# Optimization experiments

Hardware: AMD Instinct MI355X
Metric: run time of the kernel (lower is better)

The kernel has to match this reference:

```python
import jax, jax.numpy as jnp
import numpy as np

B, C_IN, C_OUT, H, W = 8, 4, 64, 8, 2048


def setup_inputs() -> dict:
    key = jax.random.key(0)
    ks = jax.random.split(key, 7)
    # torch Conv2d default init: U(-s, s) with s = 1/sqrt(fan_in), fan_in = C_in*1*1
    s = 1.0 / np.sqrt(C_IN)
    u = lambda k, shape: jax.random.uniform(k, shape, jnp.float32, -s, s)
    return {
        "x": jax.random.normal(ks[0], (B, C_IN, H, W), jnp.float32),
        "Wq": u(ks[1], (C_OUT, C_IN)), "bq": u(ks[2], (C_OUT,)),
        "Wk": u(ks[3], (C_OUT, C_IN)), "bk": u(ks[4], (C_OUT,)),
        "Wv": u(ks[5], (C_OUT, C_IN)), "bv": u(ks[6], (C_OUT,)),
        "causal": 1,
    }


def reference(x, Wq, bq, Wk, bk, Wv, bv, causal):
    b, c_in, h, w = x.shape
    # 1x1 conv == per-pixel linear over channel axis
    def proj(Wm, bm):
        y = jnp.einsum('bchw,oc->bohw', x, Wm) + bm[None, :, None, None]
        return y.reshape(b, -1, w)              # [B, C_out*H, W]
    Q = proj(Wq, bq)
    K = proj(Wk, bk)
    V = proj(Wv, bv)
    d = Q.shape[1]
    # scores[b,k,l] = sum_d Q[b,d,k] * K[b,d,l] / sqrt(d)   -> [B, W, W]
    scores = jnp.einsum('bdk,bdl->bkl', Q, K) / (float(d) ** 0.5)
    if causal:
        # faithful to torch: triu zeros lower triangle, then any zero -> -inf
        scores = jnp.triu(scores)
        scores = jnp.where(scores != 0, scores, -jnp.inf)
    attn = jax.nn.softmax(scores, axis=-1)
    # x_out[b,d,k] = sum_l V[b,d,l] * attn[b,k,l]
    x_out = jnp.einsum('bdl,bkl->bdk', V, attn).reshape(b, -1, h, w)
    return x_out, scores  # plot_weight is the pre-softmax (masked) scores
```

## Files before the change

### kernel.cpp

```cpp
#include <hip/hip_runtime.h>
#include <math.h>


#define B_ 8
#define W_ 2048
#define D_ 512
#define SCALE_ 0.04419417382415922f
#define NEG_BIG_ (-3.0e38f)

typedef __attribute__((ext_vector_type(8))) short bf16x8;
typedef __attribute__((ext_vector_type(4))) float f32x4;

__device__ __forceinline__ unsigned short f2bf(float x) {
  unsigned int u = __float_as_uint(x);
  u += 0x7fffu + ((u >> 16) & 1u);
  return (unsigned short)(u >> 16);
}
__device__ __forceinline__ float bf2f(unsigned short h) {
  return __uint_as_float(((unsigned int)h) << 16);
}
__device__ __forceinline__ void split2(float x, unsigned short& hi, unsigned short& lo) {
  hi = f2bf(x);
  lo = f2bf(x - bf2f(hi));
}

__device__ __forceinline__ void gl16(const unsigned short* g, unsigned short* l) {
  __builtin_amdgcn_global_load_lds(
      (__attribute__((address_space(1))) void*)const_cast<unsigned short*>(g),
      (__attribute__((address_space(3))) void*)l, 16, 0, 0);
}

__device__ __forceinline__ int swz(int row, int lq) {
  return row * 32 + ((lq ^ ((row >> 1) & 3)) << 3);
}

__global__ __launch_bounds__(256) void proj_all(
    const float* __restrict__ x,
    const float* __restrict__ Wq, const float* __restrict__ bq,
    const float* __restrict__ Wk, const float* __restrict__ bk,
    const float* __restrict__ Wv, const float* __restrict__ bv,
    unsigned short* __restrict__ Qhi, unsigned short* __restrict__ Qlo,
    unsigned short* __restrict__ Khi, unsigned short* __restrict__ Klo,
    unsigned short* __restrict__ Vhi, unsigned short* __restrict__ Vlo) {
  int bid = blockIdx.x;
  if (bid < 4096) {
    int idx = bid * 256 + threadIdx.x;
    int o = idx & 63;
    int w = (idx >> 6) & (W_ - 1);
    int b = idx >> 17;
    const float* xb = x + (size_t)b * 32 * W_ + w;
    float xv[4][8];
#pragma unroll
    for (int c = 0; c < 4; c++)
#pragma unroll
      for (int h = 0; h < 8; h++) xv[c][h] = xb[(c * 8 + h) * W_];
    float wq0 = Wq[o * 4], wq1 = Wq[o * 4 + 1], wq2 = Wq[o * 4 + 2], wq3 = Wq[o * 4 + 3];
    float wk0 = Wk[o * 4], wk1 = Wk[o * 4 + 1], wk2 = Wk[o * 4 + 2], wk3 = Wk[o * 4 + 3];
    float bqv = bq[o], bkv = bk[o];
    unsigned short qh8[8] __attribute__((aligned(16))), ql8[8] __attribute__((aligned(16)));
    unsigned short kh8[8] __attribute__((aligned(16))), kl8[8] __attribute__((aligned(16)));
#pragma unroll
    for (int h = 0; h < 8; h++) {
      float q = bqv + wq0 * xv[0][h] + wq1 * xv[1][h] + wq2 * xv[2][h] + wq3 * xv[3][h];
      float k = bkv + wk0 * xv[0][h] + wk1 * xv[1][h] + wk2 * xv[2][h] + wk3 * xv[3][h];
      split2(q, qh8[h], ql8[h]);
      split2(k, kh8[h], kl8[h]);
    }
    size_t base = ((size_t)b * W_ + w) * D_ + o * 8;
    *(uint4*)&Qhi[base] = *(uint4*)qh8;
    *(uint4*)&Qlo[base] = *(uint4*)ql8;
    *(uint4*)&Khi[base] = *(uint4*)kh8;
    *(uint4*)&Klo[base] = *(uint4*)kl8;
  } else {
    int idx = (bid - 4096) * 256 + threadIdx.x;
    int wc = idx & 255;
    int d = (idx >> 8) & (D_ - 1);
    int b = idx >> 17;
    int o = d >> 3, h = d & 7;
    const float* xp = x + ((size_t)(b * 4) * 8 + h) * W_ + wc * 8;
    float4 xa[4][2];
#pragma unroll
    for (int c = 0; c < 4; c++) {
      xa[c][0] = *(const float4*)&xp[(size_t)c * 8 * W_];
      xa[c][1] = *(const float4*)&xp[(size_t)c * 8 * W_ + 4];
    }
    float w0 = Wv[o * 4], w1 = Wv[o * 4 + 1], w2 = Wv[o * 4 + 2], w3 = Wv[o * 4 + 3];
    float bvv = bv[o];
    unsigned short vh8[8] __attribute__((aligned(16))), vl8[8] __attribute__((aligned(16)));
#pragma unroll
    for (int j = 0; j < 8; j++) {
      float x0 = (j < 4) ? ((const float*)&xa[0][0])[j] : ((const float*)&xa[0][1])[j - 4];
      float x1 = (j < 4) ? ((const float*)&xa[1][0])[j] : ((const float*)&xa[1][1])[j - 4];
      float x2 = (j < 4) ? ((const float*)&xa[2][0])[j] : ((const float*)&xa[2][1])[j - 4];
      float x3 = (j < 4) ? ((const float*)&xa[3][0])[j] : ((const float*)&xa[3][1])[j - 4];
      float v = bvv + w0 * x0 + w1 * x1 + w2 * x2 + w3 * x3;
      split2(v, vh8[j], vl8[j]);
    }
    size_t base = ((size_t)b * D_ + d) * W_ + wc * 8;
    *(uint4*)&Vhi[base] = *(uint4*)vh8;
    *(uint4*)&Vlo[base] = *(uint4*)vl8;
  }
}

__global__ __launch_bounds__(256) void scores_mfma(
    const unsigned short* __restrict__ Qhi, const unsigned short* __restrict__ Qlo,
    const unsigned short* __restrict__ Khi, const unsigned short* __restrict__ Klo,
    float* __restrict__ S, float2* __restrict__ stats, const int* __restrict__ causal_p) {
  int f = (blockIdx.z * 16 + blockIdx.y) * 16 + blockIdx.x;
  int lf = (f & 7) * 256 + (f >> 3);
  int b = lf >> 8;
  int k0 = ((lf >> 4) & 15) * 128;
  int l0 = (lf & 15) * 128;
  int causal = *causal_p;
  int t = threadIdx.x;
  float* Sb = S + (size_t)b * W_ * W_;

  if (causal && (l0 + 127 < k0)) {
    float4 nb = make_float4(NEG_BIG_, NEG_BIG_, NEG_BIG_, NEG_BIG_);
    int row = t >> 1, c0 = (t & 1) * 64;
#pragma unroll
    for (int j = 0; j < 16; j++)
      *(float4*)&Sb[(size_t)(k0 + row) * W_ + l0 + c0 + j * 4] = nb;
    return;
  }

  __shared__ __align__(16) unsigned short qh_s[2][4096], ql_s[2][4096];
  __shared__ __align__(16) unsigned short kh_s[2][4096], kl_s[2][4096];
  __shared__ float sm_h[2][128], ss_h[2][128];

  int wave = t >> 6, lane = t & 63;
  int wk0 = (wave >> 1) * 64, wl0 = (wave & 1) * 64;
  int lr = lane & 15, lq = lane >> 4;

  const unsigned short* Qhb = Qhi + ((size_t)b * W_ + k0) * D_;
  const unsigned short* Qlb = Qlo + ((size_t)b * W_ + k0) * D_;
  const unsigned short* Khb = Khi + ((size_t)b * W_ + l0) * D_;
  const unsigned short* Klb = Klo + ((size_t)b * W_ + l0) * D_;

  int srow0 = t >> 2, sq = t & 3;
  int srow1 = srow0 + 64;
  size_t g0 = (size_t)srow0 * D_ + ((sq ^ ((srow0 >> 1) & 3)) << 3);
  size_t g1 = (size_t)srow1 * D_ + ((sq ^ ((srow1 >> 1) & 3)) << 3);
  int a0 = t * 8, a1 = t * 8 + 2048;

  auto stage = [&](int buf, int d0) {
    gl16(Qhb + g0 + d0, &qh_s[buf][a0]);
    gl16(Qhb + g1 + d0, &qh_s[buf][a1]);
    gl16(Qlb + g0 + d0, &ql_s[buf][a0]);
    gl16(Qlb + g1 + d0, &ql_s[buf][a1]);
    gl16(Khb + g0 + d0, &kh_s[buf][a0]);
    gl16(Khb + g1 + d0, &kh_s[buf][a1]);
    gl16(Klb + g0 + d0, &kl_s[buf][a0]);
    gl16(Klb + g1 + d0, &kl_s[buf][a1]);
  };

  f32x4 acc[4][4];
#pragma unroll
  for (int i = 0; i < 4; i++)
#pragma unroll
    for (int j = 0; j < 4; j++) acc[i][j] = (f32x4){0.f, 0.f, 0.f, 0.f};

  stage(0, 0);
  __syncthreads();

  for (int i = 0; i < 16; i++) {
    int cur = i & 1;
    if (i < 15) stage(cur ^ 1, (i + 1) * 32);

    bf16x8 ah[4], al[4], bh[4], bl[4];
#pragma unroll
    for (int mt = 0; mt < 4; mt++) {
      int a = swz(wk0 + mt * 16 + lr, lq);
      ah[mt] = *(const bf16x8*)&qh_s[cur][a];
      al[mt] = *(const bf16x8*)&ql_s[cur][a];
    }
#pragma unroll
    for (int nt = 0; nt < 4; nt++) {
      int a = swz(wl0 + nt * 16 + lr, lq);
      bh[nt] = *(const bf16x8*)&kh_s[cur][a];
      bl[nt] = *(const bf16x8*)&kl_s[cur][a];
    }
    __builtin_amdgcn_s_setprio(1);
#pragma unroll
    for (int mt = 0; mt < 4; mt++)
#pragma unroll
      for (int nt = 0; nt < 4; nt++) {
        acc[mt][nt] = __builtin_amdgcn_mfma_f32_16x16x32_bf16(ah[mt], bh[nt], acc[mt][nt], 0, 0, 0);
        acc[mt][nt] = __builtin_amdgcn_mfma_f32_16x16x32_bf16(ah[mt], bl[nt], acc[mt][nt], 0, 0, 0);
        acc[mt][nt] = __builtin_amdgcn_mfma_f32_16x16x32_bf16(al[mt], bh[nt], acc[mt][nt], 0, 0, 0);
      }
    __builtin_amdgcn_s_setprio(0);
    __syncthreads();
  }

  int wh = wl0 >> 6;
#pragma unroll
  for (int mt = 0; mt < 4; mt++)
#pragma unroll
    for (int r = 0; r < 4; r++) {
      int rr = wk0 + mt * 16 + lq * 4 + r;
      int k = k0 + rr;
      float v4[4];
#pragma unroll
      for (int nt = 0; nt < 4; nt++) {
        int l = l0 + wl0 + nt * 16 + lr;
        float s = acc[mt][nt][r] * SCALE_;
        if (causal && (l < k || s == 0.0f)) s = NEG_BIG_;
        Sb[(size_t)k * W_ + l] = s;
        v4[nt] = s;
      }
      float mx = fmaxf(fmaxf(v4[0], v4[1]), fmaxf(v4[2], v4[3]));
#pragma unroll
      for (int off = 1; off < 16; off <<= 1) mx = fmaxf(mx, __shfl_xor(mx, off, 64));
      float ss = __expf(v4[0] - mx) + __expf(v4[1] - mx) +
                 __expf(v4[2] - mx) + __expf(v4[3] - mx);
#pragma unroll
      for (int off = 1; off < 16; off <<= 1) ss += __shfl_xor(ss, off, 64);
      if (lr == 0) { sm_h[wh][rr] = mx; ss_h[wh][rr] = ss; }
    }
  __syncthreads();
  if (t < 128) {
    float m0 = sm_h[0][t], m1 = sm_h[1][t];
    float s0 = ss_h[0][t], s1 = ss_h[1][t];
    float m = fmaxf(m0, m1);
    float ssum = s0 * __expf(m0 - m) + s1 * __expf(m1 - m);
    stats[((size_t)b * W_ + k0 + t) * 16 + (l0 >> 7)] = make_float2(m, ssum);
  }
}

__global__ __launch_bounds__(256) void out_bal(
    const unsigned short* __restrict__ Vhi, const unsigned short* __restrict__ Vlo,
    const float* __restrict__ S, const float2* __restrict__ stats,
    float* __restrict__ O, const int* __restrict__ causal_p) {
  int f = blockIdx.z * 64 + blockIdx.x;
  int lf = (f & 7) * 64 + (f >> 3);
  int b = lf >> 6;
  int j2 = lf & 63;
  int k0 = (j2 >> 2) * 128;
  int dq = j2 & 3;
  int causal = *causal_p;
  int t = threadIdx.x;
  int wave = t >> 6, lane = t & 63;
  int wd0 = (wave >> 1) * 64;
  int wk0 = (wave & 1) * 64;
  int lr = lane & 15, lq = lane >> 4;

  __shared__ __align__(16) unsigned short vh_s[2][128 * 32], vl_s[2][128 * 32];
  __shared__ __align__(16) unsigned short ph_s[2][128 * 32], pl_s[2][128 * 32];

  const unsigned short* Vhb = Vhi + ((size_t)b * D_ + dq * 128) * W_;
  const unsigned short* Vlb = Vlo + ((size_t)b * D_ + dq * 128) * W_;
  const float* Sb = S + (size_t)b * W_ * W_;

  int rA = t >> 2, qc = t & 3;
  int vx = (qc ^ ((rA >> 1) & 3)) << 3;
  const unsigned short* VhA = Vhb + (size_t)rA * W_ + vx;
  const unsigned short* VhB = VhA + (size_t)64 * W_;
  const unsigned short* VlA = Vlb + (size_t)rA * W_ + vx;
  const unsigned short* VlB = VlA + (size_t)64 * W_;
  int a0 = t * 8, a1 = t * 8 + 2048;

  const float* SrowA = Sb + (size_t)(k0 + rA) * W_ + qc * 8;
  const float* SrowB = SrowA + (size_t)64 * W_;
  int pA = rA * 32 + vx;
  int pB = pA + 64 * 32;

  int lt0 = causal ? (k0 >> 7) : 0;
  const float2* spA = stats + ((size_t)b * W_ + k0 + rA) * 16;
  const float2* spB = spA + 64 * 16;
  float mA = -INFINITY, mB = -INFINITY;
  for (int lt = lt0; lt < 16; lt++) mA = fmaxf(mA, spA[lt].x);
  for (int lt = lt0; lt < 16; lt++) mB = fmaxf(mB, spB[lt].x);
  float sA = 0.f, sB = 0.f;
  for (int lt = lt0; lt < 16; lt++) sA += spA[lt].y * __expf(spA[lt].x - mA);
  for (int lt = lt0; lt < 16; lt++) sB += spB[lt].y * __expf(spB[lt].x - mB);
  float iA = 1.0f / sA, iB = 1.0f / sB;

  f32x4 acc[4][4];
#pragma unroll
  for (int i = 0; i < 4; i++)
#pragma unroll
    for (int j = 0; j < 4; j++) acc[i][j] = (f32x4){0.f, 0.f, 0.f, 0.f};

  int lstart = causal ? k0 : 0;
  int nch = (W_ - lstart) >> 5;

  auto stageV = [&](int buf, int l) {
    gl16(VhA + l, &vh_s[buf][a0]);
    gl16(VhB + l, &vh_s[buf][a1]);
    gl16(VlA + l, &vl_s[buf][a0]);
    gl16(VlB + l, &vl_s[buf][a1]);
  };
  auto writeP = [&](unsigned short* __restrict__ ph, unsigned short* __restrict__ pl,
                    float4 sa0, float4 sa1, float4 sb0, float4 sb1) {
    float p[8];
    unsigned short hi8[8] __attribute__((aligned(16)));
    unsigned short lo8[8] __attribute__((aligned(16)));
    p[0] = __expf(sa0.x - mA) * iA; p[1] = __expf(sa0.y - mA) * iA;
    p[2] = __expf(sa0.z - mA) * iA; p[3] = __expf(sa0.w - mA) * iA;
    p[4] = __expf(sa1.x - mA) * iA; p[5] = __expf(sa1.y - mA) * iA;
    p[6] = __expf(sa1.z - mA) * iA; p[7] = __expf(sa1.w - mA) * iA;
#pragma unroll
    for (int j = 0; j < 8; j++) split2(p[j], hi8[j], lo8[j]);
    *(uint4*)&ph[pA] = *(uint4*)hi8;
    *(uint4*)&pl[pA] = *(uint4*)lo8;
    p[0] = __expf(sb0.x - mB) * iB; p[1] = __expf(sb0.y - mB) * iB;
    p[2] = __expf(sb0.z - mB) * iB; p[3] = __expf(sb0.w - mB) * iB;
    p[4] = __expf(sb1.x - mB) * iB; p[5] = __expf(sb1.y - mB) * iB;
    p[6] = __expf(sb1.z - mB) * iB; p[7] = __expf(sb1.w - mB) * iB;
#pragma unroll
    for (int j = 0; j < 8; j++) split2(p[j], hi8[j], lo8[j]);
    *(uint4*)&ph[pB] = *(uint4*)hi8;
    *(uint4*)&pl[pB] = *(uint4*)lo8;
  };
  auto compute = [&](const unsigned short* vh, const unsigned short* vl,
                     const unsigned short* ph, const unsigned short* pl) {
    bf16x8 ah[4], al[4], bh[4], bl[4];
#pragma unroll
    for (int mt = 0; mt < 4; mt++) {
      int a = swz(wd0 + mt * 16 + lr, lq);
      ah[mt] = *(const bf16x8*)&vh[a];
      al[mt] = *(const bf16x8*)&vl[a];
    }
#pragma unroll
    for (int nt = 0; nt < 4; nt++) {
      int a = swz(wk0 + nt * 16 + lr, lq);
      bh[nt] = *(const bf16x8*)&ph[a];
      bl[nt] = *(const bf16x8*)&pl[a];
    }
    __builtin_amdgcn_s_setprio(1);
#pragma unroll
    for (int mt = 0; mt < 4; mt++)
#pragma unroll
      for (int nt = 0; nt < 4; nt++) {
        acc[mt][nt] = __builtin_amdgcn_mfma_f32_16x16x32_bf16(ah[mt], bh[nt], acc[mt][nt], 0, 0, 0);
        acc[mt][nt] = __builtin_amdgcn_mfma_f32_16x16x32_bf16(ah[mt], bl[nt], acc[mt][nt], 0, 0, 0);
        acc[mt][nt] = __builtin_amdgcn_mfma_f32_16x16x32_bf16(al[mt], bh[nt], acc[mt][nt], 0, 0, 0);
      }
    __builtin_amdgcn_s_setprio(0);
  };

  float4 sAE0, sAE1, sBE0, sBE1, sAO0, sAO1, sBO0, sBO1;

  sAE0 = *(const float4*)&SrowA[lstart];      sAE1 = *(const float4*)&SrowA[lstart + 4];
  sBE0 = *(const float4*)&SrowB[lstart];      sBE1 = *(const float4*)&SrowB[lstart + 4];
  sAO0 = *(const float4*)&SrowA[lstart + 32]; sAO1 = *(const float4*)&SrowA[lstart + 36];
  sBO0 = *(const float4*)&SrowB[lstart + 32]; sBO1 = *(const float4*)&SrowB[lstart + 36];
  stageV(0, lstart);
  writeP(&ph_s[0][0], &pl_s[0][0], sAE0, sAE1, sBE0, sBE1);
  __syncthreads();

  for (int ci = 0; ci < nch; ci += 2) {
    int base = lstart + ci * 32;
    if (ci + 2 < nch) {
      sAE0 = *(const float4*)&SrowA[base + 64]; sAE1 = *(const float4*)&SrowA[base + 68];
      sBE0 = *(const float4*)&SrowB[base + 64]; sBE1 = *(const float4*)&SrowB[base + 68];
    }
    stageV(1, base + 32);
    writeP(&ph_s[1][0], &pl_s[1][0], sAO0, sAO1, sBO0, sBO1);
    compute(&vh_s[0][0], &vl_s[0][0], &ph_s[0][0], &pl_s[0][0]);
    __syncthreads();
    bool more = (ci + 2 < nch);
    if (ci + 3 < nch) {
      sAO0 = *(const float4*)&SrowA[base + 96]; sAO1 = *(const float4*)&SrowA[base + 100];
      sBO0 = *(const float4*)&SrowB[base + 96]; sBO1 = *(const float4*)&SrowB[base + 100];
    }
    if (more) {
      stageV(0, base + 64);
      writeP(&ph_s[0][0], &pl_s[0][0], sAE0, sAE1, sBE0, sBE1);
    }
    compute(&vh_s[1][0], &vl_s[1][0], &ph_s[1][0], &pl_s[1][0]);
    __syncthreads();
  }

#pragma unroll
  for (int mt = 0; mt < 4; mt++)
#pragma unroll
    for (int nt = 0; nt < 4; nt++)
#pragma unroll
      for (int r = 0; r < 4; r++) {
        int d = dq * 128 + wd0 + mt * 16 + lq * 4 + r;
        int k = k0 + wk0 + nt * 16 + lr;
        O[((size_t)b * D_ + d) * W_ + k] = acc[mt][nt][r];
      }
}

extern "C" void kernel_launch(void* const* d_in, const int* in_sizes, int n_in,
                              void* d_out, int out_size, void* d_ws, size_t ws_size,
                              hipStream_t stream) {
  const float* x  = (const float*)d_in[0];
  const float* Wq = (const float*)d_in[1];
  const float* bq = (const float*)d_in[2];
  const float* Wk = (const float*)d_in[3];
  const float* bk = (const float*)d_in[4];
  const float* Wv = (const float*)d_in[5];
  const float* bv = (const float*)d_in[6];
  const int* causal = (const int*)d_in[7];

  float* out = (float*)d_out;
  float* x_out = out;
  float* S = out + (size_t)B_ * D_ * W_;

  const size_t NQ = (size_t)B_ * W_ * D_;
  unsigned short* wsu = (unsigned short*)d_ws;
  unsigned short* Qhi = wsu;
  unsigned short* Qlo = wsu + NQ;
  unsigned short* Khi = wsu + 2 * NQ;
  unsigned short* Klo = wsu + 3 * NQ;
  unsigned short* Vhi = wsu + 4 * NQ;
  unsigned short* Vlo = wsu + 5 * NQ;
  float2* stats = (float2*)(wsu + 6 * NQ);

  proj_all<<<8192, 256, 0, stream>>>(x, Wq, bq, Wk, bk, Wv, bv,
                                     Qhi, Qlo, Khi, Klo, Vhi, Vlo);
  scores_mfma<<<dim3(16, 16, B_), 256, 0, stream>>>(Qhi, Qlo, Khi, Klo, S, stats, causal);
  out_bal<<<dim3(64, 1, B_), 256, 0, stream>>>(Vhi, Vlo, S, stats, x_out, causal);
}
```

Before: 371.7 us.

## Triple-buffer V loads with partial vmcnt waits; single-buffer score-kernel LDS

```diff
diff --git a/kernel.cpp b/kernel.cpp
--- a/kernel.cpp
+++ b/kernel.cpp
@@ -33,6 +33,9 @@
 __device__ __forceinline__ int swz(int row, int lq) {
   return row * 32 + ((lq ^ ((row >> 1) & 3)) << 3);
 }
+
+#define BAR_KEEP8() asm volatile("s_waitcnt vmcnt(8) lgkmcnt(0)\n\ts_barrier" ::: "memory")
+#define BAR_DRAIN() asm volatile("s_waitcnt vmcnt(0) lgkmcnt(0)\n\ts_barrier" ::: "memory")
 
 __global__ __launch_bounds__(256) void proj_all(
     const float* __restrict__ x,
@@ -124,8 +127,8 @@
     return;
   }
 
-  __shared__ __align__(16) unsigned short qh_s[2][4096], ql_s[2][4096];
-  __shared__ __align__(16) unsigned short kh_s[2][4096], kl_s[2][4096];
+  __shared__ __align__(16) unsigned short qh_s[128 * 32], ql_s[128 * 32];
+  __shared__ __align__(16) unsigned short kh_s[128 * 32], kl_s[128 * 32];
   __shared__ float sm_h[2][128], ss_h[2][128];
 
   int wave = t >> 6, lane = t & 63;
@@ -143,42 +146,35 @@
   size_t g1 = (size_t)srow1 * D_ + ((sq ^ ((srow1 >> 1) & 3)) << 3);
   int a0 = t * 8, a1 = t * 8 + 2048;
 
-  auto stage = [&](int buf, int d0) {
-    gl16(Qhb + g0 + d0, &qh_s[buf][a0]);
-    gl16(Qhb + g1 + d0, &qh_s[buf][a1]);
-    gl16(Qlb + g0 + d0, &ql_s[buf][a0]);
-    gl16(Qlb + g1 + d0, &ql_s[buf][a1]);
-    gl16(Khb + g0 + d0, &kh_s[buf][a0]);
-    gl16(Khb + g1 + d0, &kh_s[buf][a1]);
-    gl16(Klb + g0 + d0, &kl_s[buf][a0]);
-    gl16(Klb + g1 + d0, &kl_s[buf][a1]);
-  };
-
   f32x4 acc[4][4];
 #pragma unroll
   for (int i = 0; i < 4; i++)
 #pragma unroll
     for (int j = 0; j < 4; j++) acc[i][j] = (f32x4){0.f, 0.f, 0.f, 0.f};
 
-  stage(0, 0);
-  __syncthreads();
-
-  for (int i = 0; i < 16; i++) {
-    int cur = i & 1;
-    if (i < 15) stage(cur ^ 1, (i + 1) * 32);
+  for (int d0 = 0; d0 < D_; d0 += 32) {
+    gl16(Qhb + g0 + d0, &qh_s[a0]);
+    gl16(Qhb + g1 + d0, &qh_s[a1]);
+    gl16(Qlb + g0 + d0, &ql_s[a0]);
+    gl16(Qlb + g1 + d0, &ql_s[a1]);
+    gl16(Khb + g0 + d0, &kh_s[a0]);
+    gl16(Khb + g1 + d0, &kh_s[a1]);
+    gl16(Klb + g0 + d0, &kl_s[a0]);
+    gl16(Klb + g1 + d0, &kl_s[a1]);
+    __syncthreads();
 
     bf16x8 ah[4], al[4], bh[4], bl[4];
 #pragma unroll
     for (int mt = 0; mt < 4; mt++) {
       int a = swz(wk0 + mt * 16 + lr, lq);
-      ah[mt] = *(const bf16x8*)&qh_s[cur][a];
-      al[mt] = *(const bf16x8*)&ql_s[cur][a];
+      ah[mt] = *(const bf16x8*)&qh_s[a];
+      al[mt] = *(const bf16x8*)&ql_s[a];
     }
 #pragma unroll
     for (int nt = 0; nt < 4; nt++) {
       int a = swz(wl0 + nt * 16 + lr, lq);
-      bh[nt] = *(const bf16x8*)&kh_s[cur][a];
-      bl[nt] = *(const bf16x8*)&kl_s[cur][a];
+      bh[nt] = *(const bf16x8*)&kh_s[a];
+      bl[nt] = *(const bf16x8*)&kl_s[a];
     }
     __builtin_amdgcn_s_setprio(1);
 #pragma unroll
@@ -245,8 +241,8 @@
   int wk0 = (wave & 1) * 64;
   int lr = lane & 15, lq = lane >> 4;
 
-  __shared__ __align__(16) unsigned short vh_s[2][128 * 32], vl_s[2][128 * 32];
-  __shared__ __align__(16) unsigned short ph_s[2][128 * 32], pl_s[2][128 * 32];
+  __shared__ __align__(16) unsigned short vh_s[3][4096], vl_s[3][4096];
+  __shared__ __align__(16) unsigned short ph_s[2][4096], pl_s[2][4096];
 
   const unsigned short* Vhb = Vhi + ((size_t)b * D_ + dq * 128) * W_;
   const unsigned short* Vlb = Vlo + ((size_t)b * D_ + dq * 128) * W_;
@@ -285,11 +281,16 @@
   int lstart = causal ? k0 : 0;
   int nch = (W_ - lstart) >> 5;
 
-  auto stageV = [&](int buf, int l) {
-    gl16(VhA + l, &vh_s[buf][a0]);
-    gl16(VhB + l, &vh_s[buf][a1]);
-    gl16(VlA + l, &vl_s[buf][a0]);
-    gl16(VlB + l, &vl_s[buf][a1]);
+  unsigned short *vhR = &vh_s[0][0], *vhN = &vh_s[1][0], *vhT = &vh_s[2][0];
+  unsigned short *vlR = &vl_s[0][0], *vlN = &vl_s[1][0], *vlT = &vl_s[2][0];
+  unsigned short *phC = &ph_s[0][0], *plC = &pl_s[0][0];
+  unsigned short *phN = &ph_s[1][0], *plN = &pl_s[1][0];
+
+  auto stageV = [&](unsigned short* vh, unsigned short* vl, int l) {
+    gl16(VhA + l, &vh[a0]);
+    gl16(VhB + l, &vh[a1]);
+    gl16(VlA + l, &vl[a0]);
+    gl16(VlB + l, &vl[a1]);
   };
   auto writeP = [&](unsigned short* __restrict__ ph, unsigned short* __restrict__ pl,
                     float4 sa0, float4 sa1, float4 sb0, float4 sb1) {
@@ -339,38 +340,46 @@
       }
     __builtin_amdgcn_s_setprio(0);
   };
+  auto rotV = [&]() {
+    unsigned short* th = vhR; vhR = vhN; vhN = vhT; vhT = th;
+    unsigned short* tl = vlR; vlR = vlN; vlN = vlT; vlT = tl;
+    unsigned short* tp = phC; phC = phN; phN = tp;
+    unsigned short* tq = plC; plC = plN; plN = tq;
+  };
 
   float4 sAE0, sAE1, sBE0, sBE1, sAO0, sAO1, sBO0, sBO1;
 
+  stageV(vhR, vlR, lstart);
+  stageV(vhN, vlN, lstart + 32);
   sAE0 = *(const float4*)&SrowA[lstart];      sAE1 = *(const float4*)&SrowA[lstart + 4];
   sBE0 = *(const float4*)&SrowB[lstart];      sBE1 = *(const float4*)&SrowB[lstart + 4];
   sAO0 = *(const float4*)&SrowA[lstart + 32]; sAO1 = *(const float4*)&SrowA[lstart + 36];
   sBO0 = *(const float4*)&SrowB[lstart + 32]; sBO1 = *(const float4*)&SrowB[lstart + 36];
-  stageV(0, lstart);
-  writeP(&ph_s[0][0], &pl_s[0][0], sAE0, sAE1, sBE0, sBE1);
+  writeP(phC, plC, sAE0, sAE1, sBE0, sBE1);
   __syncthreads();
 
   for (int ci = 0; ci < nch; ci += 2) {
     int base = lstart + ci * 32;
-    if (ci + 2 < nch) {
+    bool s2 = (ci + 2 < nch);
+    if (s2) {
+      stageV(vhT, vlT, base + 64);
       sAE0 = *(const float4*)&SrowA[base + 64]; sAE1 = *(const float4*)&SrowA[base + 68];
       sBE0 = *(const float4*)&SrowB[base + 64]; sBE1 = *(const float4*)&SrowB[base + 68];
     }
-    stageV(1, base + 32);
-    writeP(&ph_s[1][0], &pl_s[1][0], sAO0, sAO1, sBO0, sBO1);
-    compute(&vh_s[0][0], &vl_s[0][0], &ph_s[0][0], &pl_s[0][0]);
-    __syncthreads();
-    bool more = (ci + 2 < nch);
-    if (ci + 3 < nch) {
+    writeP(phN, plN, sAO0, sAO1, sBO0, sBO1);
+    compute(vhR, vlR, phC, plC);
+    if (s2) BAR_KEEP8(); else BAR_DRAIN();
+    rotV();
+    bool s3 = (ci + 3 < nch);
+    if (s3) {
+      stageV(vhT, vlT, base + 96);
       sAO0 = *(const float4*)&SrowA[base + 96]; sAO1 = *(const float4*)&SrowA[base + 100];
       sBO0 = *(const float4*)&SrowB[base + 96]; sBO1 = *(const float4*)&SrowB[base + 100];
     }
-    if (more) {
-      stageV(0, base + 64);
-      writeP(&ph_s[0][0], &pl_s[0][0], sAE0, sAE1, sBE0, sBE1);
-    }
-    compute(&vh_s[1][0], &vl_s[1][0], &ph_s[1][0], &pl_s[1][0]);
-    __syncthreads();
+    if (s2) writeP(phN, plN, sAE0, sAE1, sBE0, sBE1);
+    compute(vhR, vlR, phC, plC);
+    if (s3) BAR_KEEP8(); else BAR_DRAIN();
+    rotV();
   }
 
 #pragma unroll
```

After: 398.8 us. 1.07x slower.

## Reorder causal tile dispatch and single-buffer LDS staging in scores kernel

Applied to the files above, without the earlier changes.

```diff
diff --git a/kernel.cpp b/kernel.cpp
--- a/kernel.cpp
+++ b/kernel.cpp
@@ -107,11 +107,25 @@
     const unsigned short* __restrict__ Khi, const unsigned short* __restrict__ Klo,
     float* __restrict__ S, float2* __restrict__ stats, const int* __restrict__ causal_p) {
   int f = (blockIdx.z * 16 + blockIdx.y) * 16 + blockIdx.x;
-  int lf = (f & 7) * 256 + (f >> 3);
-  int b = lf >> 8;
-  int k0 = ((lf >> 4) & 15) * 128;
-  int l0 = (lf & 15) * 128;
+  int b = f & 7;
+  int r = f >> 3;
   int causal = *causal_p;
+  int k0idx, l0idx;
+  if (causal) {
+    if (r < 136) {
+      int xx = r, k = 0;
+      while (xx >= 16 - k) { xx -= 16 - k; k++; }
+      k0idx = k; l0idx = k + xx;
+    } else {
+      int xx = r - 136, k = 1;
+      while (xx >= k) { xx -= k; k++; }
+      k0idx = k; l0idx = xx;
+    }
+  } else {
+    k0idx = r >> 4; l0idx = r & 15;
+  }
+  int k0 = k0idx * 128;
+  int l0 = l0idx * 128;
   int t = threadIdx.x;
   float* Sb = S + (size_t)b * W_ * W_;
 
@@ -124,8 +138,8 @@
     return;
   }
 
-  __shared__ __align__(16) unsigned short qh_s[2][4096], ql_s[2][4096];
-  __shared__ __align__(16) unsigned short kh_s[2][4096], kl_s[2][4096];
+  __shared__ __align__(16) unsigned short qh_s[128 * 32], ql_s[128 * 32];
+  __shared__ __align__(16) unsigned short kh_s[128 * 32], kl_s[128 * 32];
   __shared__ float sm_h[2][128], ss_h[2][128];
 
   int wave = t >> 6, lane = t & 63;
@@ -143,42 +157,35 @@
   size_t g1 = (size_t)srow1 * D_ + ((sq ^ ((srow1 >> 1) & 3)) << 3);
   int a0 = t * 8, a1 = t * 8 + 2048;
 
-  auto stage = [&](int buf, int d0) {
-    gl16(Qhb + g0 + d0, &qh_s[buf][a0]);
-    gl16(Qhb + g1 + d0, &qh_s[buf][a1]);
-    gl16(Qlb + g0 + d0, &ql_s[buf][a0]);
-    gl16(Qlb + g1 + d0, &ql_s[buf][a1]);
-    gl16(Khb + g0 + d0, &kh_s[buf][a0]);
-    gl16(Khb + g1 + d0, &kh_s[buf][a1]);
-    gl16(Klb + g0 + d0, &kl_s[buf][a0]);
-    gl16(Klb + g1 + d0, &kl_s[buf][a1]);
-  };
-
   f32x4 acc[4][4];
 #pragma unroll
   for (int i = 0; i < 4; i++)
 #pragma unroll
     for (int j = 0; j < 4; j++) acc[i][j] = (f32x4){0.f, 0.f, 0.f, 0.f};
 
-  stage(0, 0);
-  __syncthreads();
-
-  for (int i = 0; i < 16; i++) {
-    int cur = i & 1;
-    if (i < 15) stage(cur ^ 1, (i + 1) * 32);
+  for (int d0 = 0; d0 < D_; d0 += 32) {
+    gl16(Qhb + g0 + d0, &qh_s[a0]);
+    gl16(Qhb + g1 + d0, &qh_s[a1]);
+    gl16(Qlb + g0 + d0, &ql_s[a0]);
+    gl16(Qlb + g1 + d0, &ql_s[a1]);
+    gl16(Khb + g0 + d0, &kh_s[a0]);
+    gl16(Khb + g1 + d0, &kh_s[a1]);
+    gl16(Klb + g0 + d0, &kl_s[a0]);
+    gl16(Klb + g1 + d0, &kl_s[a1]);
+    __syncthreads();
 
     bf16x8 ah[4], al[4], bh[4], bl[4];
 #pragma unroll
     for (int mt = 0; mt < 4; mt++) {
       int a = swz(wk0 + mt * 16 + lr, lq);
-      ah[mt] = *(const bf16x8*)&qh_s[cur][a];
-      al[mt] = *(const bf16x8*)&ql_s[cur][a];
+      ah[mt] = *(const bf16x8*)&qh_s[a];
+      al[mt] = *(const bf16x8*)&ql_s[a];
     }
 #pragma unroll
     for (int nt = 0; nt < 4; nt++) {
       int a = swz(wl0 + nt * 16 + lr, lq);
-      bh[nt] = *(const bf16x8*)&kh_s[cur][a];
-      bl[nt] = *(const bf16x8*)&kl_s[cur][a];
+      bh[nt] = *(const bf16x8*)&kh_s[a];
+      bl[nt] = *(const bf16x8*)&kl_s[a];
     }
     __builtin_amdgcn_s_setprio(1);
 #pragma unroll
@@ -197,14 +204,14 @@
 #pragma unroll
   for (int mt = 0; mt < 4; mt++)
 #pragma unroll
-    for (int r = 0; r < 4; r++) {
-      int rr = wk0 + mt * 16 + lq * 4 + r;
+    for (int r2 = 0; r2 < 4; r2++) {
+      int rr = wk0 + mt * 16 + lq * 4 + r2;
       int k = k0 + rr;
       float v4[4];
 #pragma unroll
       for (int nt = 0; nt < 4; nt++) {
         int l = l0 + wl0 + nt * 16 + lr;
-        float s = acc[mt][nt][r] * SCALE_;
+        float s = acc[mt][nt][r2] * SCALE_;
         if (causal && (l < k || s == 0.0f)) s = NEG_BIG_;
         Sb[(size_t)k * W_ + l] = s;
         v4[nt] = s;
@@ -233,11 +240,12 @@
     const float* __restrict__ S, const float2* __restrict__ stats,
     float* __restrict__ O, const int* __restrict__ causal_p) {
   int f = blockIdx.z * 64 + blockIdx.x;
-  int lf = (f & 7) * 64 + (f >> 3);
-  int b = lf >> 6;
-  int j2 = lf & 63;
-  int k0 = (j2 >> 2) * 128;
-  int dq = j2 & 3;
+  int b = f & 7;
+  int xx = f >> 3;
+  int k0idx, dq;
+  if (xx < 32) { k0idx = xx >> 2;              dq = xx & 3; }
+  else         { k0idx = 15 - ((xx - 32) >> 2); dq = (xx - 32) & 3; }
+  int k0 = k0idx * 128;
   int causal = *causal_p;
   int t = threadIdx.x;
   int wave = t >> 6, lane = t & 63;
```

After: 402.1 us. +8.2%, slower.
